# Kernel tuning notes

Hardware: AMD Instinct MI355X
Metric: run time of the kernel (lower is better)

## Reference

```python
import jax, jax.numpy as jnp
import numpy as np

# Fixed reactor dimensions and grey-box constants (from hyb_greybox_pars / xuyscales)
NX, NU, NY, NP = 3, 1, 2, 4
NZ = NP * (NY + NU)          # 12
F, V, DELTA = 0.1, 1.0, 1.0
CAMEAN, CBMEAN = 1.0, 0.5    # yscale mean
CASTD, CBSTD = 0.5, 0.3      # yscale std
CAFMEAN, CAFSTD = 2.0, 0.5   # uscale


def _fnn(x, layers):
    """Feed-forward NN: tanh hidden layers, linear output layer."""
    for W, b in layers[:-1]:
        x = jnp.tanh(x @ W + b)
    W, b = layers[-1]
    return x @ W + b


def setup_inputs() -> dict:
    key = jax.random.key(0)
    ks = jax.random.split(key, 16)
    B, T = 2048, 1024
    d = {
        "useq": jax.random.normal(ks[0], (B, T, NU), jnp.float32),
        "x0": 0.1 * jax.random.normal(ks[1], (B, NX + NZ), jnp.float32),
    }
    s1 = 1.0 / np.sqrt(1.0)
    s16 = 1.0 / np.sqrt(16.0)
    s12 = 1.0 / np.sqrt(12.0)
    s32 = 1.0 / np.sqrt(32.0)
    for i, name in enumerate(["r1", "r2", "r3"]):
        d[name + "_W0"] = s1 * jax.random.normal(ks[2 + 2 * i], (1, 16), jnp.float32)
        d[name + "_b0"] = jnp.zeros((16,), jnp.float32)
        d[name + "_W1"] = s16 * jax.random.normal(ks[3 + 2 * i], (16, 1), jnp.float32)
        d[name + "_b1"] = jnp.zeros((1,), jnp.float32)
    d["estC_W0"] = s12 * jax.random.normal(ks[10], (12, 32), jnp.float32)
    d["estC_b0"] = jnp.zeros((32,), jnp.float32)
    d["estC_W1"] = s32 * jax.random.normal(ks[11], (32, 1), jnp.float32)
    d["estC_b1"] = jnp.zeros((1,), jnp.float32)
    return d


def reference(useq, x0,
              r1_W0, r1_b0, r1_W1, r1_b1,
              r2_W0, r2_b0, r2_W1, r2_b1,
              r3_W0, r3_b0, r3_W1, r3_b1,
              estC_W0, estC_b0, estC_W1, estC_b1):
    r1L = [(r1_W0, r1_b0), (r1_W1, r1_b1)]
    r2L = [(r2_W0, r2_b0), (r2_W1, r2_b1)]
    r3L = [(r3_W0, r3_b0), (r3_W1, r3_b1)]
    estCL = [(estC_W0, estC_b0), (estC_W1, estC_b1)]

    def fxu(x, u):
        Ca, Cb, Cc = x[:, 0:1], x[:, 1:2], x[:, 2:3]
        Caf = u[:, 0:1]
        r1 = _fnn(Ca, r1L) * CASTD
        r2 = _fnn(Cb, r2L) * CBSTD
        r3 = _fnn(Cc, r3L) * CBSTD
        Ca = Ca * CASTD + CAMEAN
        Cb = Cb * CBSTD + CBMEAN
        Cc = Cc * CBSTD + CBMEAN
        Caf = Caf * CAFSTD + CAFMEAN
        dCa = F * (Caf - Ca) / V - r1
        dCb = -F * Cb / V + r1 - 3.0 * r2 + r3
        dCc = -F * Cc / V + r2 - r3
        return jnp.concatenate([dCa / CASTD, dCb / CBSTD, dCc / CBSTD], axis=-1)

    def step(xz, u):
        x, z = xz[:, :NX], xz[:, NX:]
        ypseq, upseq = z[:, :NP * NY], z[:, NP * NY:]
        k1 = fxu(x, u)
        k2 = fxu(x + DELTA * (k1 / 2.0), u)
        k3 = fxu(x + DELTA * (k2 / 2.0), u)
        k4 = fxu(x + DELTA * k3, u)
        xplus = x + (DELTA / 6.0) * (k1 + 2.0 * k2 + 2.0 * k3 + k4)
        zplus = jnp.concatenate([ypseq[:, NY:], x[:, :NY], upseq[:, NU:], u], axis=-1)
        CcNN = _fnn(z, estCL)
        y = jnp.concatenate([x, CcNN], axis=-1)   # [B, Ny + 2*numUnmeasGb] = [B, 4]
        return jnp.concatenate([xplus, zplus], axis=-1), y

    u_t = jnp.swapaxes(useq, 0, 1)                # [T, B, Nu]
    _, ys = jax.lax.scan(step, x0, u_t)           # ys: [T, B, 4]
    return jnp.swapaxes(ys, 0, 1)                 # [B, T, 4]
```

## Files before the change

### kernel.cpp

```cpp
#include <hip/hip_runtime.h>

#define TT 1024
#define BB 2048
#define L2E2 2.8853900817779268f

typedef float v2f __attribute__((ext_vector_type(2)));

template <int CTRL>
__device__ __forceinline__ float dpp_add(float x) {
  int y = __builtin_amdgcn_update_dpp(0, __float_as_int(x), CTRL, 0xF, 0xF, true);
  return x + __int_as_float(y);
}
template <int CTRL>
__device__ __forceinline__ float dpp_mov(float x) {
  int y = __builtin_amdgcn_update_dpp(0, __float_as_int(x), CTRL, 0xF, 0xF, true);
  return __int_as_float(y);
}
__device__ __forceinline__ float sum8(float x) {
  x = dpp_add<0xB1>(x);
  x = dpp_add<0x4E>(x);
  x = dpp_add<0x141>(x);
  return x;
}
__device__ __forceinline__ float rdlane(float x, int l) {
  return __int_as_float(__builtin_amdgcn_readlane(__float_as_int(x), l));
}

__global__ __launch_bounds__(256) void phase1_kernel(
    const float* __restrict__ useq, const float* __restrict__ x0,
    const float* __restrict__ r1W0, const float* __restrict__ r1b0,
    const float* __restrict__ r1W1, const float* __restrict__ r1b1,
    const float* __restrict__ r2W0, const float* __restrict__ r2b0,
    const float* __restrict__ r2W1, const float* __restrict__ r2b1,
    const float* __restrict__ r3W0, const float* __restrict__ r3b0,
    const float* __restrict__ r3W1, const float* __restrict__ r3b1,
    const float* __restrict__ eW0, const float* __restrict__ eb0p,
    const float* __restrict__ eW1, const float* __restrict__ eb1p,
    float* __restrict__ out) {
  const int lane = threadIdx.x & 63;
  const int eh = lane >> 5;
  const int g = (lane >> 3) & 3;
  const int i = lane & 7;
  const int e0 = __builtin_amdgcn_readfirstlane(
      (blockIdx.x * 4 + (threadIdx.x >> 6)) * 2);
  const int e = e0 + eh;

  const float* W0p = (g == 3) ? r2W0 : (g == 2) ? r3W0 : r1W0;
  const float* b0p = (g == 3) ? r2b0 : (g == 2) ? r3b0 : r1b0;
  const float* W1p = (g == 3) ? r2W1 : (g == 2) ? r3W1 : r1W1;

  const v2f w0s = {W0p[i] * L2E2, W0p[i + 8] * L2E2};
  const v2f b0s = {b0p[i] * L2E2, b0p[i + 8] * L2E2};
  const v2f iwn = {1.0f / (-2.0f * W1p[i]),
                   1.0f / (-2.0f * W1p[i + 8])};

  float C1 = r1b1[0], C2 = r2b1[0], C3 = r3b1[0];
  for (int q = 0; q < 16; ++q) {
    C1 += r1W1[q];
    C2 += r2W1[q];
    C3 += r3W1[q];
  }
  const float caC = 0.2f - C1;
  const float cbC = -1.0f / 6.0f + (5.0f / 3.0f) * C1 - 3.0f * C2 + C3;
  const float ccC = -1.0f / 6.0f + C2 - C3;

  const int strow = (g <= 1) ? 0 : (g == 2) ? 2 : 1;
  const float cstBase = (g == 3) ? cbC : (g == 2) ? ccC : caC;
  const float uco = (g <= 1) ? 0.1f : 0.0f;
  const float c_own = (g == 3) ? -3.0f : -1.0f;
  const float c_qr = (g >= 2) ? 1.0f : 0.0f;
  const float c_m2 = (g == 3) ? (5.0f / 3.0f) : 0.0f;

  float S = x0[e * 15 + strow];

  const int n = lane & 31;
  const float eb0v = eb0p[n] * L2E2;
  const float ew0 = eW0[0 * 32 + n] * L2E2;
  const float ew1 = eW0[1 * 32 + n] * L2E2;
  const float ew2 = eW0[2 * 32 + n] * L2E2;
  const float ew3 = eW0[3 * 32 + n] * L2E2;
  const float ew4 = eW0[4 * 32 + n] * L2E2;
  const float ew5 = eW0[5 * 32 + n] * L2E2;
  const float ew6 = eW0[6 * 32 + n] * L2E2;
  const float ew7 = eW0[7 * 32 + n] * L2E2;
  const float ew8 = eW0[8 * 32 + n] * L2E2;
  const float ew9 = eW0[9 * 32 + n] * L2E2;
  const float ew10 = eW0[10 * 32 + n] * L2E2;
  const float ew11 = eW0[11 * 32 + n] * L2E2;
  const float ew1n = -2.0f * eW1[n];
  float ebs = eb1p[0];
  for (int q = 0; q < 32; ++q) ebs += eW1[q];
  const float eb32 = ebs * 0.03125f;

  const float* zp = x0 + e * 15 + 3;
  float hA0 = zp[0], hB0 = zp[1], hA1 = zp[2], hB1 = zp[3];
  float hA2 = zp[4], hB2 = zp[5], hA3 = zp[6], hB3 = zp[7];
  float hU0 = zp[8], hU1 = zp[9], hU2 = zp[10], hU3 = zp[11];

  const float* up0 = useq + e0 * TT;
  const float* up1 = useq + (e0 + 1) * TT;
  const int l31 = lane & 31;
  const int soff = (l31 == 0) ? 0 : (l31 == 24) ? 1 : (l31 == 16) ? 2 : 3;
  float* op = out + (size_t)e * TT * 4 + soff;
  const bool sflag = (l31 == 0) | (l31 == 24) | (l31 == 16) | (l31 == 17);
  const bool isE = (l31 == 17);

#define STAGE(SS, KK)                                                     \
  {                                                                       \
    v2f h = __builtin_elementwise_fma(w0s, (v2f){(SS), (SS)}, b0s);       \
    h.x = __builtin_amdgcn_exp2f(h.x);                                    \
    h.y = __builtin_amdgcn_exp2f(h.y);                                    \
    h = __builtin_elementwise_fma(h, iwn, iwn);                           \
    float rv = __builtin_amdgcn_rcpf(h.x) + __builtin_amdgcn_rcpf(h.y);   \
    float q = sum8(rv);                                                   \
    float qr = dpp_mov<0x128>(q);           \
    float m2 = dpp_mov<0x142>(q);     \
    float t_ = fmaf(-0.1f, (SS), cstS);                                   \
    t_ = fmaf(c_own, q, t_);                                              \
    t_ = fmaf(c_qr, qr, t_);                                              \
    KK = fmaf(c_m2, m2, t_);                                              \
  }

#define STEP(UA, UB, SC_, hA0_, hB0_, hA1_, hB1_, hA2_, hB2_, hA3_, hB3_, \
             hU0_, hU1_, hU2_, hU3_, NA_, NB_, NU_)                       \
  {                                                                       \
    float a_ = fmaf((hA0_), ew0, eb0v);                                   \
    a_ = fmaf((hB0_), ew1, a_);                                           \
    a_ = fmaf((hA1_), ew2, a_);                                           \
    a_ = fmaf((hB1_), ew3, a_);                                           \
    a_ = fmaf((hA2_), ew4, a_);                                           \
    a_ = fmaf((hB2_), ew5, a_);                                           \
    a_ = fmaf((hA3_), ew6, a_);                                           \
    a_ = fmaf((hB3_), ew7, a_);                                           \
    a_ = fmaf((hU0_), ew8, a_);                                           \
    a_ = fmaf((hU1_), ew9, a_);                                           \
    a_ = fmaf((hU2_), ew10, a_);                                          \
    a_ = fmaf((hU3_), ew11, a_);                                          \
    float er_ = __builtin_amdgcn_rcpf(__builtin_amdgcn_exp2f(a_) + 1.0f); \
    float ps_ = fmaf(ew1n, er_, eb32);                                    \
    ps_ = dpp_add<0xB1>(ps_);                                             \
    ps_ = dpp_add<0x4E>(ps_);                                             \
    ps_ = dpp_add<0x141>(ps_);                                            \
    ps_ = dpp_add<0x140>(ps_);                       \
    ps_ = dpp_add<0x142>(ps_);         \
    const float sAa_ = rdlane(S, 0);                                      \
    const float sBa_ = rdlane(S, 24);                                     \
    const float sAb_ = rdlane(S, 32);                                     \
    const float sBb_ = rdlane(S, 56);                                     \
    NA_ = eh ? sAb_ : sAa_;                                               \
    NB_ = eh ? sBb_ : sBa_;                                               \
    const float usel_ = eh ? (UB) : (UA);                                 \
    NU_ = usel_;                                                          \
    const float cstS = fmaf(uco, usel_, cstBase);                         \
    SC_ = isE ? ps_ : S;                                                  \
    float k1, k2, k3, k4;                                                 \
    STAGE(S, k1)                                                          \
    float s2 = fmaf(0.5f, k1, S);                                         \
    STAGE(s2, k2)                                                         \
    float s3 = fmaf(0.5f, k2, S);                                         \
    STAGE(s3, k3)                                                         \
    float s4 = S + k3;                                                    \
    STAGE(s4, k4)                                                         \
    S = fmaf(1.0f / 6.0f, fmaf(2.0f, k2 + k3, k1) + k4, S);               \
  }

  float4 cura = *(const float4*)(up0);
  float4 curb = *(const float4*)(up1);

  for (int t0 = 0; t0 < TT; t0 += 4) {
    const int tn = (t0 + 4 <= TT - 4) ? (t0 + 4) : (TT - 4);
    const float4 naa = *(const float4*)(up0 + tn);
    const float4 nab = *(const float4*)(up1 + tn);

    float sc0, sc1, sc2, sc3;
    float A4, B4, U4, A5, B5, U5, A6, B6, U6, A7, B7, U7;
    STEP(cura.x, curb.x, sc0, hA0, hB0, hA1, hB1, hA2, hB2, hA3, hB3,
         hU0, hU1, hU2, hU3, A4, B4, U4)
    STEP(cura.y, curb.y, sc1, hA1, hB1, hA2, hB2, hA3, hB3, A4, B4,
         hU1, hU2, hU3, U4, A5, B5, U5)
    STEP(cura.z, curb.z, sc2, hA2, hB2, hA3, hB3, A4, B4, A5, B5,
         hU2, hU3, U4, U5, A6, B6, U6)
    STEP(cura.w, curb.w, sc3, hA3, hB3, A4, B4, A5, B5, A6, B6,
         hU3, U4, U5, U6, A7, B7, U7)

    if (sflag) {
      float* p = op + t0 * 4;
      p[0] = sc0;  p[4] = sc1;  p[8] = sc2;  p[12] = sc3;
    }

    hA0 = A4; hB0 = B4; hA1 = A5; hB1 = B5;
    hA2 = A6; hB2 = B6; hA3 = A7; hB3 = B7;
    hU0 = U4; hU1 = U5; hU2 = U6; hU3 = U7;

    cura = naa;
    curb = nab;
  }
#undef STEP
#undef STAGE
}

extern "C" void kernel_launch(void* const* d_in, const int* in_sizes, int n_in,
                              void* d_out, int out_size, void* d_ws,
                              size_t ws_size, hipStream_t stream) {
  const float* useq = (const float*)d_in[0];
  const float* x0 = (const float*)d_in[1];
  float* out = (float*)d_out;

  phase1_kernel<<<BB / 8, 256, 0, stream>>>(
      useq, x0,
      (const float*)d_in[2], (const float*)d_in[3], (const float*)d_in[4],
      (const float*)d_in[5], (const float*)d_in[6], (const float*)d_in[7],
      (const float*)d_in[8], (const float*)d_in[9], (const float*)d_in[10],
      (const float*)d_in[11], (const float*)d_in[12], (const float*)d_in[13],
      (const float*)d_in[14], (const float*)d_in[15], (const float*)d_in[16],
      (const float*)d_in[17], out);
}
```

Baseline: 383.0 us.

## Unroll time loop to 8 steps and replace two readlanes with row DPP broadcast

Unrolls the serial time loop from 4 to 8 steps per iteration, loading two float4 chunks of the control input per row and storing 8 outputs per flush. The Ca history update now uses a row-broadcast DPP move instead of two readlane calls plus a select. The RK4 combine is also regrouped into a 1/3 and 1/6 FMA form. These changes aim to cut loop overhead, readlane latency and dependent arithmetic on the recurrence critical path, at the cost of more registers and a small floating-point rounding difference.

New measurement: 386.8 us. About the same (+1.0%).

```diff
diff --git a/kernel.cpp b/kernel.cpp
--- a/kernel.cpp
+++ b/kernel.cpp
@@ -104,6 +104,7 @@
   float* op = out + (size_t)e * TT * 4 + soff;
   const bool sflag = (l31 == 0) | (l31 == 24) | (l31 == 16) | (l31 == 17);
   const bool isE = (l31 == 17);
+  const bool loRow = (l31 < 16);
 
 #define STAGE(SS, KK)                                                     \
   {                                                                       \
@@ -143,11 +144,9 @@
     ps_ = dpp_add<0x141>(ps_);                                            \
     ps_ = dpp_add<0x140>(ps_);                       \
     ps_ = dpp_add<0x142>(ps_);         \
-    const float sAa_ = rdlane(S, 0);                                      \
+    NA_ = loRow ? S : dpp_mov<0x142>(S);    \
     const float sBa_ = rdlane(S, 24);                                     \
-    const float sAb_ = rdlane(S, 32);                                     \
     const float sBb_ = rdlane(S, 56);                                     \
-    NA_ = eh ? sAb_ : sAa_;                                               \
     NB_ = eh ? sBb_ : sBa_;                                               \
     const float usel_ = eh ? (UB) : (UA);                                 \
     NU_ = usel_;                                                          \
@@ -161,39 +160,52 @@
     STAGE(s3, k3)                                                         \
     float s4 = S + k3;                                                    \
     STAGE(s4, k4)                                                         \
-    S = fmaf(1.0f / 6.0f, fmaf(2.0f, k2 + k3, k1) + k4, S);               \
-  }
-
-  float4 cura = *(const float4*)(up0);
-  float4 curb = *(const float4*)(up1);
-
-  for (int t0 = 0; t0 < TT; t0 += 4) {
-    const int tn = (t0 + 4 <= TT - 4) ? (t0 + 4) : (TT - 4);
-    const float4 naa = *(const float4*)(up0 + tn);
-    const float4 nab = *(const float4*)(up1 + tn);
-
-    float sc0, sc1, sc2, sc3;
+    S = fmaf(1.0f / 6.0f, k1 + k4, fmaf(1.0f / 3.0f, k2 + k3, S));        \
+  }
+
+  float4 ca0 = *(const float4*)(up0);
+  float4 ca1 = *(const float4*)(up0 + 4);
+  float4 cb0 = *(const float4*)(up1);
+  float4 cb1 = *(const float4*)(up1 + 4);
+
+  for (int t0 = 0; t0 < TT; t0 += 8) {
+    const int tn = (t0 + 8 <= TT - 8) ? (t0 + 8) : (TT - 8);
+    const float4 na0 = *(const float4*)(up0 + tn);
+    const float4 na1 = *(const float4*)(up0 + tn + 4);
+    const float4 nb0 = *(const float4*)(up1 + tn);
+    const float4 nb1 = *(const float4*)(up1 + tn + 4);
+
+    float sc0, sc1, sc2, sc3, sc4, sc5, sc6, sc7;
     float A4, B4, U4, A5, B5, U5, A6, B6, U6, A7, B7, U7;
-    STEP(cura.x, curb.x, sc0, hA0, hB0, hA1, hB1, hA2, hB2, hA3, hB3,
+    float A8, B8, U8, A9, B9, U9, A10, B10, U10, A11, B11, U11;
+    STEP(ca0.x, cb0.x, sc0, hA0, hB0, hA1, hB1, hA2, hB2, hA3, hB3,
          hU0, hU1, hU2, hU3, A4, B4, U4)
-    STEP(cura.y, curb.y, sc1, hA1, hB1, hA2, hB2, hA3, hB3, A4, B4,
+    STEP(ca0.y, cb0.y, sc1, hA1, hB1, hA2, hB2, hA3, hB3, A4, B4,
          hU1, hU2, hU3, U4, A5, B5, U5)
-    STEP(cura.z, curb.z, sc2, hA2, hB2, hA3, hB3, A4, B4, A5, B5,
+    STEP(ca0.z, cb0.z, sc2, hA2, hB2, hA3, hB3, A4, B4, A5, B5,
          hU2, hU3, U4, U5, A6, B6, U6)
-    STEP(cura.w, curb.w, sc3, hA3, hB3, A4, B4, A5, B5, A6, B6,
+    STEP(ca0.w, cb0.w, sc3, hA3, hB3, A4, B4, A5, B5, A6, B6,
          hU3, U4, U5, U6, A7, B7, U7)
+    STEP(ca1.x, cb1.x, sc4, A4, B4, A5, B5, A6, B6, A7, B7,
+         U4, U5, U6, U7, A8, B8, U8)
+    STEP(ca1.y, cb1.y, sc5, A5, B5, A6, B6, A7, B7, A8, B8,
+         U5, U6, U7, U8, A9, B9, U9)
+    STEP(ca1.z, cb1.z, sc6, A6, B6, A7, B7, A8, B8, A9, B9,
+         U6, U7, U8, U9, A10, B10, U10)
+    STEP(ca1.w, cb1.w, sc7, A7, B7, A8, B8, A9, B9, A10, B10,
+         U7, U8, U9, U10, A11, B11, U11)
 
     if (sflag) {
       float* p = op + t0 * 4;
-      p[0] = sc0;  p[4] = sc1;  p[8] = sc2;  p[12] = sc3;
+      p[0] = sc0;   p[4] = sc1;   p[8] = sc2;   p[12] = sc3;
+      p[16] = sc4;  p[20] = sc5;  p[24] = sc6;  p[28] = sc7;
     }
 
-    hA0 = A4; hB0 = B4; hA1 = A5; hB1 = B5;
-    hA2 = A6; hB2 = B6; hA3 = A7; hB3 = B7;
-    hU0 = U4; hU1 = U5; hU2 = U6; hU3 = U7;
-
-    cura = naa;
-    curb = nab;
+    hA0 = A8;  hB0 = B8;  hA1 = A9;  hB1 = B9;
+    hA2 = A10; hB2 = B10; hA3 = A11; hB3 = B11;
+    hU0 = U8;  hU1 = U9;  hU2 = U10; hU3 = U11;
+
+    ca0 = na0; ca1 = na1; cb0 = nb0; cb1 = nb1;
   }
 #undef STEP
 #undef STAGE
```
